# Kernel optimization log

Hardware: AMD Instinct MI355X
Metric: run time of the kernel (lower is better)

The kernel has to match this reference:

```python
import jax, jax.numpy as jnp
import numpy as np

P = 16            # num_patches = 224 // 14
T = P * P         # patches per image (256)
K = 5             # top-k templates
SIM_THR = 0.05
PATCH_THR = 2.0


def _idx2loc(idx):
    # flat patch index -> (w, h) float location, matching convert_index2location
    return jnp.stack([(idx % P).astype(jnp.float32), (idx // P).astype(jnp.float32)], axis=-1)


def setup_inputs() -> dict:
    key = jax.random.key(0)
    k1, k2, k3, k4 = jax.random.split(key, 4)
    B, N, C = 8, 32, 768
    src_feats = jax.random.normal(k1, (B, N, C, P, P), dtype=jnp.float32)
    tar_feat = jax.random.normal(k2, (B, C, P, P), dtype=jnp.float32)
    src_masks = (jax.random.uniform(k3, (B, N, P, P)) > 0.3).astype(jnp.float32)
    tar_mask = (jax.random.uniform(k4, (B, P, P)) > 0.3).astype(jnp.float32)
    return {"src_feats": src_feats, "tar_feat": tar_feat,
            "src_masks": src_masks, "tar_mask": tar_mask}


def reference(src_feats, tar_feat, src_masks, tar_mask):
    B, N, C = src_feats.shape[:3]
    # masks are already at feature resolution -> interpolate is identity; flatten
    tarm = tar_mask.reshape(B, T)                                   # (B, T)
    srcm = src_masks.reshape(B, N, T)                               # (B, N, T)
    # L2-normalize features over channel dim (F.normalize)
    tf = tar_feat / jnp.clip(jnp.linalg.norm(tar_feat, axis=1, keepdims=True), 1e-12)
    tf = tf.reshape(B, C, T)                                        # (B, C, T)
    sf = src_feats / jnp.clip(jnp.linalg.norm(src_feats, axis=2, keepdims=True), 1e-12)
    sf = sf.reshape(B, N, C, T)                                     # (B, N, C, S)
    # dense cosine similarity, masked, then thresholded to 0
    sim = jnp.einsum('bct,bncs->bnts', tf, sf)                      # (B, N, T, S)
    sim = sim * srcm[:, :, None, :] * tarm[:, None, :, None]
    sim = jnp.where(sim < SIM_THR, 0.0, sim)
    # dual nearest-neighbor search ('tar2src' direction)
    score_t2s = sim.max(axis=3)                                     # (B, N, T)
    idx_t2s = sim.argmax(axis=3).astype(jnp.int32)
    score_s2t = sim.max(axis=2)                                     # (B, N, S)
    idx_s2t = sim.argmax(axis=2).astype(jnp.int32)
    mask_sim = score_t2s >= SIM_THR
    # cycle consistency: tar -> src -> tar
    idx_s2s = jnp.take_along_axis(idx_s2t, idx_t2s, axis=2)         # (B, N, T)
    dist = jnp.linalg.norm(_idx2loc(idx_s2s) - _idx2loc(jnp.arange(T))[None, None], axis=-1)
    sim_s2s = jnp.take_along_axis(score_s2t, idx_t2s, axis=2)
    mask_cycle = (dist <= PATCH_THR) & (sim_s2s >= SIM_THR)
    # non-zero / in-mask filtering
    mask_t2s = jnp.take_along_axis(srcm, idx_t2s, axis=2)           # (B, N, T)
    mask_nz = tarm[:, None, :] * mask_t2s * (idx_s2t != 0) * (idx_t2s != 0)
    mask_all = (mask_sim & mask_cycle) * mask_nz                    # (B, N, T) float
    match_counts = mask_all.sum(axis=2)                             # (B, N)
    sim_avg = jnp.where(match_counts > 0,
                        (score_t2s * mask_all).sum(axis=2) / float(T), 0.0)
    # top-k template selection
    score_src, id_src = jax.lax.top_k(sim_avg, K)                   # (B, K)
    sel = lambda a: jnp.take_along_axis(a, id_src[:, :, None], axis=1)
    pred_mask = sel(mask_all)                                       # (B, K, T)
    score_pts = sel(score_t2s)                                      # (B, K, T)
    src_loc = _idx2loc(sel(idx_t2s)).astype(jnp.int32)              # (B, K, T, 2)
    # format_prediction: -1 outside mask, (w, h) coords inside
    grid = _idx2loc(jnp.arange(T)).astype(jnp.int32)                # (T, 2)
    nz = (pred_mask != 0)[..., None]
    tar_pts = jnp.where(nz, grid[None, None], -1)                   # (B, K, T, 2)
    src_pts = jnp.where(nz, src_loc, -1)                            # (B, K, T, 2)
    return id_src, score_src, score_pts, tar_pts, src_pts, match_counts
```

## Files before the change

kernel.cpp:

```cpp
#include <hip/hip_runtime.h>

#define T_PATCH 256
#define C_DIM   768
#define NCH     48
#define N_B     8
#define N_N     32

typedef unsigned short u16;
typedef u16   u16x8  __attribute__((ext_vector_type(8)));
typedef short s16x8  __attribute__((ext_vector_type(8)));
typedef float f32x16 __attribute__((ext_vector_type(16)));

__device__ __forceinline__ unsigned rne16(unsigned u) {
    return (u + 0x7fffu + ((u >> 16) & 1u)) >> 16;
}

__device__ __forceinline__ void split3(float x, u16& o0, u16& o1, u16& o2) {
    unsigned u0 = rne16(__float_as_uint(x));
    float f0 = __uint_as_float(u0 << 16);
    float r1 = x - f0;
    unsigned u1 = rne16(__float_as_uint(r1));
    float f1 = __uint_as_float(u1 << 16);
    float r2 = r1 - f1;
    o0 = (u16)u0; o1 = (u16)u1; o2 = (u16)(__float_as_uint(r2) >> 16);
}

__global__ void tar_split_kernel(const float* __restrict__ tar,
                                 u16* __restrict__ tS0, u16* __restrict__ tS1,
                                 u16* __restrict__ tS2, float* __restrict__ partT) {
    int blk = blockIdx.x;
    int b = blk / NCH, c = blk - b * NCH;
    int tid = threadIdx.x;
    int g = tid >> 8, t = tid & 255;
    const float* tb = tar + (size_t)b * C_DIM * T_PATCH;
    float ss = 0.f;
    u16x8 v0, v1, v2;
    #pragma unroll
    for (int j = 0; j < 8; ++j) {
        float x = tb[(c * 16 + g * 8 + j) * T_PATCH + t];
        u16 a, bb, cc;
        split3(x, a, bb, cc);
        v0[j] = a; v1[j] = bb; v2[j] = cc;
        ss = fmaf(x, x, ss);
    }
    size_t off = ((size_t)blk * 512 + tid) * 8;
    *(u16x8*)(tS0 + off) = v0;
    *(u16x8*)(tS1 + off) = v1;
    *(u16x8*)(tS2 + off) = v2;
    __shared__ float sq[512];
    sq[tid] = ss;
    __syncthreads();
    if (tid < 256) partT[blk * 256 + tid] = sq[tid] + sq[tid + 256];
}

__global__ void invt_kernel(const float* __restrict__ partT,
                            const float* __restrict__ tar_mask,
                            float* __restrict__ w_invT) {
    int b = blockIdx.x, t = threadIdx.x;
    float s = 0.f;
    for (int c = 0; c < NCH; ++c) s += partT[(b * NCH + c) * 256 + t];
    float tm = tar_mask[b * 256 + t];
    w_invT[b * 256 + t] = (tm != 0.f) ? 1.f / fmaxf(sqrtf(s), 1e-12f) : 0.f;
}

__launch_bounds__(512, 4)
__global__ void sim_kernel(const float* __restrict__ src_feats,
                           const u16* __restrict__ tS0, const u16* __restrict__ tS1,
                           const u16* __restrict__ tS2,
                           const float* __restrict__ w_invT,
                           const float* __restrict__ src_masks,
                           float* __restrict__ w_rowv, int* __restrict__ w_rowi,
                           float* __restrict__ w_s2tv, int* __restrict__ w_s2ti) {
    __shared__ __align__(16) u16 B0[2][2][128][8], B1[2][2][128][8], B2[2][2][128][8];
    __shared__ float sqS[2][128];
    __shared__ float rowv[2][256]; __shared__ int rowi[2][256];
    __shared__ float colv[4][128]; __shared__ int coli[4][128];
    __shared__ float invT[256], invS[128];

    int bh = blockIdx.x;
    int b    = bh & 7;
    int loc  = bh >> 3;
    int n    = loc >> 1;
    int half = loc & 1;
    int bn   = b * N_N + n;
    int lbh  = bn * 2 + half;

    int tid = threadIdx.x;
    int lane = tid & 63, w = tid >> 6;
    int wm = w >> 1, wn = w & 1;
    int h = lane >> 5, l5 = lane & 31;
    int colB = tid & 127, gB = (tid >> 7) & 1;

    const float* sB = src_feats + (size_t)bn * C_DIM * T_PATCH
                    + (size_t)gB * 8 * T_PATCH + half * 128 + colB;
    size_t aoff = ((size_t)b * NCH) * 4096 + (size_t)(h * 256 + wm * 64 + l5) * 8;
    const u16* pa0 = tS0 + aoff;
    const u16* pa1 = tS1 + aoff;
    const u16* pa2 = tS2 + aoff;

    if (tid < 256) invT[tid] = w_invT[b * 256 + tid];

    f32x16 acc[2][2];
    #pragma unroll
    for (int i = 0; i < 2; ++i)
        #pragma unroll
        for (int j = 0; j < 2; ++j) acc[i][j] = (f32x16)0.0f;

    float sss = 0.f;

    if (tid < 256) {
        u16x8 b0v, b1v, b2v;
        #pragma unroll
        for (int j = 0; j < 8; ++j) {
            float x = sB[j * T_PATCH];
            u16 a, bb, cc;
            split3(x, a, bb, cc);
            b0v[j] = a; b1v[j] = bb; b2v[j] = cc;
            sss = fmaf(x, x, sss);
        }
        ((u16x8*)B0[0])[tid] = b0v;
        ((u16x8*)B1[0])[tid] = b1v;
        ((u16x8*)B2[0])[tid] = b2v;
    }
    const float* psrc = sB + 4096;
    __syncthreads();

    for (int c = 0; c < NCH; ++c) {
        int p = c & 1;
        s16x8 a0[2], a1[2], a2[2];
        #pragma unroll
        for (int i = 0; i < 2; ++i) {
            a0[i] = *(const s16x8*)(pa0 + i * 256);
            a1[i] = *(const s16x8*)(pa1 + i * 256);
            a2[i] = *(const s16x8*)(pa2 + i * 256);
        }
        pa0 += 4096; pa1 += 4096; pa2 += 4096;

        float yv[8];
        bool pf = (c < NCH - 1);
        if (tid < 256 && pf) {
            #pragma unroll
            for (int j = 0; j < 8; ++j) yv[j] = psrc[j * T_PATCH];
            psrc += 4096;
        }

        __builtin_amdgcn_s_setprio(1);
        #pragma unroll
        for (int j = 0; j < 2; ++j) {
            int cl = wn * 64 + j * 32 + l5;
            s16x8 b0 = *(const s16x8*)&B0[p][h][cl][0];
            s16x8 b1 = *(const s16x8*)&B1[p][h][cl][0];
            s16x8 b2 = *(const s16x8*)&B2[p][h][cl][0];
            #pragma unroll
            for (int i = 0; i < 2; ++i) {
                acc[i][j] = __builtin_amdgcn_mfma_f32_32x32x16_bf16(a0[i], b0, acc[i][j], 0, 0, 0);
                acc[i][j] = __builtin_amdgcn_mfma_f32_32x32x16_bf16(a0[i], b1, acc[i][j], 0, 0, 0);
                acc[i][j] = __builtin_amdgcn_mfma_f32_32x32x16_bf16(a1[i], b0, acc[i][j], 0, 0, 0);
                acc[i][j] = __builtin_amdgcn_mfma_f32_32x32x16_bf16(a1[i], b1, acc[i][j], 0, 0, 0);
                acc[i][j] = __builtin_amdgcn_mfma_f32_32x32x16_bf16(a0[i], b2, acc[i][j], 0, 0, 0);
                acc[i][j] = __builtin_amdgcn_mfma_f32_32x32x16_bf16(a2[i], b0, acc[i][j], 0, 0, 0);
            }
        }
        __builtin_amdgcn_s_setprio(0);

        if (tid < 256 && pf) {
            u16x8 b0v, b1v, b2v;
            #pragma unroll
            for (int j = 0; j < 8; ++j) {
                u16 a, bb, cc;
                split3(yv[j], a, bb, cc);
                b0v[j] = a; b1v[j] = bb; b2v[j] = cc;
                sss = fmaf(yv[j], yv[j], sss);
            }
            ((u16x8*)B0[p ^ 1])[tid] = b0v;
            ((u16x8*)B1[p ^ 1])[tid] = b1v;
            ((u16x8*)B2[p ^ 1])[tid] = b2v;
        }
        __syncthreads();
    }

    if (tid < 256) ((float*)sqS)[tid] = sss;
    __syncthreads();
    if (tid < 128) {
        float ns = sqrtf(sqS[0][tid] + sqS[1][tid]);
        float smv = src_masks[bn * 256 + half * 128 + tid];
        invS[tid] = (smv != 0.f) ? 1.f / fmaxf(ns, 1e-12f) : 0.f;
    }
    __syncthreads();

    float isv[2]; int sgl[2];
    #pragma unroll
    for (int j = 0; j < 2; ++j) {
        isv[j] = invS[wn * 64 + j * 32 + l5];
        sgl[j] = half * 128 + wn * 64 + j * 32 + l5;
    }
    float cbv[2]; int cbi[2];
    #pragma unroll
    for (int j = 0; j < 2; ++j) { cbv[j] = -1.f; cbi[j] = 0; }

    #pragma unroll
    for (int i = 0; i < 2; ++i) {
        #pragma unroll
        for (int r = 0; r < 16; ++r) {
            int trow = wm * 64 + i * 32 + (r & 3) + 8 * (r >> 2) + 4 * h;
            float it = invT[trow];
            float v[2];
            #pragma unroll
            for (int j = 0; j < 2; ++j) {
                float x = acc[i][j][r] * it * isv[j];
                v[j] = (x >= 0.05f) ? x : 0.f;
            }
            float bv = -1.f; int bi = 0;
            #pragma unroll
            for (int j = 0; j < 2; ++j)
                if (v[j] > bv) { bv = v[j]; bi = sgl[j]; }
            #pragma unroll
            for (int off = 1; off < 32; off <<= 1) {
                float ov = __shfl_xor(bv, off, 64);
                int   oi = __shfl_xor(bi, off, 64);
                if (ov > bv || (ov == bv && oi < bi)) { bv = ov; bi = oi; }
            }
            if (l5 == 0) { rowv[wn][trow] = bv; rowi[wn][trow] = bi; }
            #pragma unroll
            for (int j = 0; j < 2; ++j)
                if (v[j] > cbv[j]) { cbv[j] = v[j]; cbi[j] = trow; }
        }
    }
    #pragma unroll
    for (int j = 0; j < 2; ++j) {
        float bv = cbv[j]; int bi = cbi[j];
        float ov = __shfl_xor(bv, 32, 64);
        int   oi = __shfl_xor(bi, 32, 64);
        if (ov > bv || (ov == bv && oi < bi)) { bv = ov; bi = oi; }
        if (h == 0) { colv[wm][wn * 64 + j * 32 + l5] = bv; coli[wm][wn * 64 + j * 32 + l5] = bi; }
    }
    __syncthreads();
    if (tid < 256) {
        float v0 = rowv[0][tid]; int i0 = rowi[0][tid];
        float v1 = rowv[1][tid]; int i1 = rowi[1][tid];
        if (v1 > v0 || (v1 == v0 && i1 < i0)) { v0 = v1; i0 = i1; }
        w_rowv[lbh * 256 + tid] = v0;
        w_rowi[lbh * 256 + tid] = i0;
    }
    if (tid < 128) {
        float bv = colv[0][tid]; int bi = coli[0][tid];
        #pragma unroll
        for (int q = 1; q < 4; ++q) {
            float ov = colv[q][tid]; int oi = coli[q][tid];
            if (ov > bv || (ov == bv && oi < bi)) { bv = ov; bi = oi; }
        }
        w_s2tv[bn * 256 + half * 128 + tid] = bv;
        w_s2ti[bn * 256 + half * 128 + tid] = bi;
    }
}

__global__ void combine_kernel(const float* __restrict__ w_rowv, const int* __restrict__ w_rowi,
                               const float* __restrict__ w_s2tv, const int* __restrict__ w_s2ti,
                               const float* __restrict__ src_masks, const float* __restrict__ tar_mask,
                               float* __restrict__ w_score, float* __restrict__ w_mall,
                               float* __restrict__ w_savg, int* __restrict__ w_idx,
                               float* __restrict__ out) {
    int bn = blockIdx.x; int b = bn >> 5; int t = threadIdx.x;
    __shared__ float sc_s2t[256]; __shared__ int ix_s2t[256];
    __shared__ float sm[256];
    __shared__ float red[8];
    sc_s2t[t] = w_s2tv[bn * 256 + t];
    ix_s2t[t] = w_s2ti[bn * 256 + t];
    sm[t]     = src_masks[bn * 256 + t];
    float v0 = w_rowv[(bn * 2) * 256 + t];     int i0 = w_rowi[(bn * 2) * 256 + t];
    float v1 = w_rowv[(bn * 2 + 1) * 256 + t]; int i1 = w_rowi[(bn * 2 + 1) * 256 + t];
    float st2s; int i;
    if (v1 > v0 || (v1 == v0 && i1 < i0)) { st2s = v1; i = i1; }
    else                                  { st2s = v0; i = i0; }
    float tmv = tar_mask[b * 256 + t];
    __syncthreads();

    bool msim = st2s >= 0.05f;
    int is2s = ix_s2t[i];
    int dw = (is2s & 15) - (t & 15);
    int dh = (is2s >> 4) - (t >> 4);
    bool cyc = (dw * dw + dh * dh <= 4) && (sc_s2t[i] >= 0.05f);
    float mnz = tmv * sm[i] *
                ((ix_s2t[t] != 0) ? 1.f : 0.f) *
                ((i != 0) ? 1.f : 0.f);
    float mall = (msim && cyc) ? mnz : 0.f;
    w_score[bn * 256 + t] = st2s;
    w_mall[bn * 256 + t]  = mall;
    w_idx[bn * 256 + t]   = i;

    float cnt = mall, svs = st2s * mall;
    #pragma unroll
    for (int off = 1; off < 64; off <<= 1) {
        cnt += __shfl_xor(cnt, off, 64);
        svs += __shfl_xor(svs, off, 64);
    }
    if ((t & 63) == 0) {
        red[(t >> 6) * 2]     = cnt;
        red[(t >> 6) * 2 + 1] = svs;
    }
    __syncthreads();
    if (t == 0) {
        float c = red[0] + red[2] + red[4] + red[6];
        float s = red[1] + red[3] + red[5] + red[7];
        w_savg[bn] = (c > 0.f) ? (s * (1.f / 256.f)) : 0.f;
        out[51280 + bn] = c;
    }
}

__global__ void final_kernel(const float* __restrict__ w_score,
                             const float* __restrict__ w_mall,
                             const float* __restrict__ w_savg,
                             const int*   __restrict__ w_idx,
                             float* __restrict__ out) {
    int b = blockIdx.x, tid = threadIdx.x;
    __shared__ float savg[32];
    __shared__ int   topid[5];
    __shared__ float topv[5];
    if (tid < 32) savg[tid] = w_savg[b * 32 + tid];
    __syncthreads();
    if (tid == 0) {
        unsigned used = 0;
        for (int k = 0; k < 5; ++k) {
            float bv = -1e30f; int bi = 0;
            for (int n = 0; n < 32; ++n) {
                if (!((used >> n) & 1u) && savg[n] > bv) { bv = savg[n]; bi = n; }
            }
            used |= (1u << bi);
            topid[k] = bi; topv[k] = bv;
        }
    }
    __syncthreads();
    if (tid < 5) {
        out[b * 5 + tid]      = (float)topid[tid];
        out[40 + b * 5 + tid] = topv[tid];
    }
    int t = tid;
    for (int k = 0; k < 5; ++k) {
        int bn = b * 32 + topid[k];
        float sc = w_score[bn * 256 + t];
        float ma = w_mall[bn * 256 + t];
        int   ii = w_idx[bn * 256 + t];
        int o = (b * 5 + k) * 256 + t;
        out[80 + o] = sc;
        bool nz = (ma != 0.f);
        out[10320 + 2 * o]     = nz ? (float)(t & 15)  : -1.f;
        out[10320 + 2 * o + 1] = nz ? (float)(t >> 4)  : -1.f;
        out[30800 + 2 * o]     = nz ? (float)(ii & 15) : -1.f;
        out[30800 + 2 * o + 1] = nz ? (float)(ii >> 4) : -1.f;
    }
}

extern "C" void kernel_launch(void* const* d_in, const int* in_sizes, int n_in,
                              void* d_out, int out_size, void* d_ws, size_t ws_size,
                              hipStream_t stream) {
    const float* src_feats = (const float*)d_in[0];
    const float* tar_feat  = (const float*)d_in[1];
    const float* src_masks = (const float*)d_in[2];
    const float* tar_mask  = (const float*)d_in[3];
    float* out = (float*)d_out;

    const size_t PLANE = (size_t)N_B * NCH * 512 * 8;
    u16* tS0 = (u16*)d_ws;
    u16* tS1 = tS0 + PLANE;
    u16* tS2 = tS1 + PLANE;
    float* partT  = (float*)(tS2 + PLANE);
    float* w_invT = partT + (size_t)N_B * NCH * 256;
    float* w_rowv = w_invT + 2048;
    int*   w_rowi = (int*)(w_rowv + 512 * 256);
    float* w_s2tv = (float*)(w_rowi + 512 * 256);
    int*   w_s2ti = (int*)(w_s2tv + 256 * 256);
    float* w_score = (float*)(w_s2ti + 256 * 256);
    float* w_mall  = w_score + 256 * 256;
    float* w_savg  = w_mall + 256 * 256;
    int*   w_idx   = (int*)(w_savg + 256);

    tar_split_kernel<<<N_B * NCH, 512, 0, stream>>>(tar_feat, tS0, tS1, tS2, partT);
    invt_kernel<<<N_B, 256, 0, stream>>>(partT, tar_mask, w_invT);
    sim_kernel<<<N_B * N_N * 2, 512, 0, stream>>>(src_feats, tS0, tS1, tS2, w_invT,
                                                  src_masks,
                                                  w_rowv, w_rowi, w_s2tv, w_s2ti);
    combine_kernel<<<N_B * N_N, 256, 0, stream>>>(w_rowv, w_rowi, w_s2tv, w_s2ti,
                                                  src_masks, tar_mask,
                                                  w_score, w_mall, w_savg, w_idx, out);
    final_kernel<<<N_B, 256, 0, stream>>>(w_score, w_mall, w_savg, w_idx, out);
}
```

Before: 391.8 us.

## Stage target A-tiles in LDS via async global_load_lds and split B-fill across all threads

The sim kernel now copies the pre-split target bf16 tiles straight from global memory into double-buffered LDS with global_load_lds, one 16-byte load per thread per split. Before, each wave read them from global into registers inside the MFMA loop. The source-feature split work is spread over all 512 threads at 4 channels each, where only 256 threads handled 8 each, and the norm partials are reduced over four groups. This aims to overlap A-tile fetches with compute and halve per-thread conversion latency. The cost is roughly 72KB of LDS per block, which may limit occupancy below the launch-bounds target of 4 blocks.

```diff
diff --git a/kernel.cpp b/kernel.cpp
--- a/kernel.cpp
+++ b/kernel.cpp
@@ -8,6 +8,7 @@
 
 typedef unsigned short u16;
 typedef u16   u16x8  __attribute__((ext_vector_type(8)));
+typedef u16   u16x4  __attribute__((ext_vector_type(4)));
 typedef short s16x8  __attribute__((ext_vector_type(8)));
 typedef float f32x16 __attribute__((ext_vector_type(16)));
 
@@ -23,6 +24,12 @@
     float f1 = __uint_as_float(u1 << 16);
     float r2 = r1 - f1;
     o0 = (u16)u0; o1 = (u16)u1; o2 = (u16)(__float_as_uint(r2) >> 16);
+}
+
+__device__ __forceinline__ void gll16(const u16* g, u16* l) {
+    __builtin_amdgcn_global_load_lds(
+        (const __attribute__((address_space(1))) unsigned int*)g,
+        (__attribute__((address_space(3))) unsigned int*)l, 16, 0, 0);
 }
 
 __global__ void tar_split_kernel(const float* __restrict__ tar,
@@ -71,11 +78,20 @@
                            const float* __restrict__ src_masks,
                            float* __restrict__ w_rowv, int* __restrict__ w_rowi,
                            float* __restrict__ w_s2tv, int* __restrict__ w_s2ti) {
-    __shared__ __align__(16) u16 B0[2][2][128][8], B1[2][2][128][8], B2[2][2][128][8];
-    __shared__ float sqS[2][128];
-    __shared__ float rowv[2][256]; __shared__ int rowi[2][256];
-    __shared__ float colv[4][128]; __shared__ int coli[4][128];
-    __shared__ float invT[256], invS[128];
+    __shared__ __align__(16) u16 SM[36864];
+    u16* Af0 = SM;
+    u16* Af1 = SM + 8192;
+    u16* Af2 = SM + 16384;
+    u16* Bf0 = SM + 24576;
+    u16* Bf1 = SM + 28672;
+    u16* Bf2 = SM + 32768;
+    float* sqv  = (float*)(SM);
+    float* rowv = (float*)(SM + 1024);
+    int*   rowi = (int*)  (SM + 3072);
+    float* colv = (float*)(SM + 5120);
+    int*   coli = (int*)  (SM + 6144);
+    float* invT = (float*)(SM + 7168);
+    float* invS = (float*)(SM + 7680);
 
     int bh = blockIdx.x;
     int b    = bh & 7;
@@ -89,16 +105,15 @@
     int lane = tid & 63, w = tid >> 6;
     int wm = w >> 1, wn = w & 1;
     int h = lane >> 5, l5 = lane & 31;
-    int colB = tid & 127, gB = (tid >> 7) & 1;
-
-    const float* sB = src_feats + (size_t)bn * C_DIM * T_PATCH
-                    + (size_t)gB * 8 * T_PATCH + half * 128 + colB;
-    size_t aoff = ((size_t)b * NCH) * 4096 + (size_t)(h * 256 + wm * 64 + l5) * 8;
-    const u16* pa0 = tS0 + aoff;
-    const u16* pa1 = tS1 + aoff;
-    const u16* pa2 = tS2 + aoff;
-
-    if (tid < 256) invT[tid] = w_invT[b * 256 + tid];
+    int colB = tid & 127, qB = tid >> 7;
+    int gq = qB >> 1, quad = qB & 1;
+
+    const float* psrc = src_feats + (size_t)bn * C_DIM * T_PATCH
+                      + (size_t)(gq * 8 + quad * 4) * T_PATCH + half * 128 + colB;
+    size_t abase = (size_t)b * NCH * 4096 + (size_t)tid * 8;
+    const u16* pga0 = tS0 + abase;
+    const u16* pga1 = tS1 + abase;
+    const u16* pga2 = tS2 + abase;
 
     f32x16 acc[2][2];
     #pragma unroll
@@ -108,49 +123,67 @@
 
     float sss = 0.f;
 
-    if (tid < 256) {
-        u16x8 b0v, b1v, b2v;
-        #pragma unroll
-        for (int j = 0; j < 8; ++j) {
-            float x = sB[j * T_PATCH];
+    {
+        float yv[4];
+        #pragma unroll
+        for (int j = 0; j < 4; ++j) yv[j] = psrc[j * T_PATCH];
+        psrc += 4096;
+        gll16(pga0, Af0 + tid * 8);
+        gll16(pga1, Af1 + tid * 8);
+        gll16(pga2, Af2 + tid * 8);
+        pga0 += 4096; pga1 += 4096; pga2 += 4096;
+        u16x4 b0v, b1v, b2v;
+        #pragma unroll
+        for (int j = 0; j < 4; ++j) {
             u16 a, bb, cc;
-            split3(x, a, bb, cc);
+            split3(yv[j], a, bb, cc);
             b0v[j] = a; b1v[j] = bb; b2v[j] = cc;
-            sss = fmaf(x, x, sss);
-        }
-        ((u16x8*)B0[0])[tid] = b0v;
-        ((u16x8*)B1[0])[tid] = b1v;
-        ((u16x8*)B2[0])[tid] = b2v;
-    }
-    const float* psrc = sB + 4096;
+            sss = fmaf(yv[j], yv[j], sss);
+        }
+        int bslot = (gq * 128 + colB) * 8 + quad * 4;
+        *(u16x4*)(Bf0 + bslot) = b0v;
+        *(u16x4*)(Bf1 + bslot) = b1v;
+        *(u16x4*)(Bf2 + bslot) = b2v;
+    }
     __syncthreads();
 
     for (int c = 0; c < NCH; ++c) {
         int p = c & 1;
+        bool pf = (c < NCH - 1);
+
+        float yv[4];
+        if (pf) {
+            #pragma unroll
+            for (int j = 0; j < 4; ++j) yv[j] = psrc[j * T_PATCH];
+            psrc += 4096;
+        }
+        if (pf) {
+            int adst = (p ^ 1) * 4096 + tid * 8;
+            gll16(pga0, Af0 + adst);
+            gll16(pga1, Af1 + adst);
+            gll16(pga2, Af2 + adst);
+            pga0 += 4096; pga1 += 4096; pga2 += 4096;
+        }
+
+        __builtin_amdgcn_s_setprio(1);
         s16x8 a0[2], a1[2], a2[2];
-        #pragma unroll
-        for (int i = 0; i < 2; ++i) {
-            a0[i] = *(const s16x8*)(pa0 + i * 256);
-            a1[i] = *(const s16x8*)(pa1 + i * 256);
-            a2[i] = *(const s16x8*)(pa2 + i * 256);
-        }
-        pa0 += 4096; pa1 += 4096; pa2 += 4096;
-
-        float yv[8];
-        bool pf = (c < NCH - 1);
-        if (tid < 256 && pf) {
-            #pragma unroll
-            for (int j = 0; j < 8; ++j) yv[j] = psrc[j * T_PATCH];
-            psrc += 4096;
-        }
-
-        __builtin_amdgcn_s_setprio(1);
+        {
+            const u16* Ab = Af0 + p * 4096 + (h * 256 + wm * 64 + l5) * 8;
+            #pragma unroll
+            for (int i = 0; i < 2; ++i) a0[i] = *(const s16x8*)(Ab + i * 256);
+            Ab = Af1 + p * 4096 + (h * 256 + wm * 64 + l5) * 8;
+            #pragma unroll
+            for (int i = 0; i < 2; ++i) a1[i] = *(const s16x8*)(Ab + i * 256);
+            Ab = Af2 + p * 4096 + (h * 256 + wm * 64 + l5) * 8;
+            #pragma unroll
+            for (int i = 0; i < 2; ++i) a2[i] = *(const s16x8*)(Ab + i * 256);
+        }
         #pragma unroll
         for (int j = 0; j < 2; ++j) {
-            int cl = wn * 64 + j * 32 + l5;
-            s16x8 b0 = *(const s16x8*)&B0[p][h][cl][0];
-            s16x8 b1 = *(const s16x8*)&B1[p][h][cl][0];
-            s16x8 b2 = *(const s16x8*)&B2[p][h][cl][0];
+            int boff = p * 2048 + (h * 128 + wn * 64 + j * 32 + l5) * 8;
+            s16x8 b0 = *(const s16x8*)(Bf0 + boff);
+            s16x8 b1 = *(const s16x8*)(Bf1 + boff);
+            s16x8 b2 = *(const s16x8*)(Bf2 + boff);
             #pragma unroll
             for (int i = 0; i < 2; ++i) {
                 acc[i][j] = __builtin_amdgcn_mfma_f32_32x32x16_bf16(a0[i], b0, acc[i][j], 0, 0, 0);
@@ -163,26 +196,28 @@
         }
         __builtin_amdgcn_s_setprio(0);
 
-        if (tid < 256 && pf) {
-            u16x8 b0v, b1v, b2v;
-            #pragma unroll
-            for (int j = 0; j < 8; ++j) {
+        if (pf) {
+            u16x4 b0v, b1v, b2v;
+            #pragma unroll
+            for (int j = 0; j < 4; ++j) {
                 u16 a, bb, cc;
                 split3(yv[j], a, bb, cc);
                 b0v[j] = a; b1v[j] = bb; b2v[j] = cc;
                 sss = fmaf(yv[j], yv[j], sss);
             }
-            ((u16x8*)B0[p ^ 1])[tid] = b0v;
-            ((u16x8*)B1[p ^ 1])[tid] = b1v;
-            ((u16x8*)B2[p ^ 1])[tid] = b2v;
+            int bslot = (p ^ 1) * 2048 + (gq * 128 + colB) * 8 + quad * 4;
+            *(u16x4*)(Bf0 + bslot) = b0v;
+            *(u16x4*)(Bf1 + bslot) = b1v;
+            *(u16x4*)(Bf2 + bslot) = b2v;
         }
         __syncthreads();
     }
 
-    if (tid < 256) ((float*)sqS)[tid] = sss;
+    sqv[tid] = sss;
+    if (tid < 256) invT[tid] = w_invT[b * 256 + tid];
     __syncthreads();
     if (tid < 128) {
-        float ns = sqrtf(sqS[0][tid] + sqS[1][tid]);
+        float ns = sqrtf(sqv[tid] + sqv[tid + 128] + sqv[tid + 256] + sqv[tid + 384]);
         float smv = src_masks[bn * 256 + half * 128 + tid];
         invS[tid] = (smv != 0.f) ? 1.f / fmaxf(ns, 1e-12f) : 0.f;
     }
@@ -220,7 +255,7 @@
                 int   oi = __shfl_xor(bi, off, 64);
                 if (ov > bv || (ov == bv && oi < bi)) { bv = ov; bi = oi; }
             }
-            if (l5 == 0) { rowv[wn][trow] = bv; rowi[wn][trow] = bi; }
+            if (l5 == 0) { rowv[wn * 256 + trow] = bv; rowi[wn * 256 + trow] = bi; }
             #pragma unroll
             for (int j = 0; j < 2; ++j)
                 if (v[j] > cbv[j]) { cbv[j] = v[j]; cbi[j] = trow; }
@@ -232,21 +267,22 @@
         float ov = __shfl_xor(bv, 32, 64);
         int   oi = __shfl_xor(bi, 32, 64);
         if (ov > bv || (ov == bv && oi < bi)) { bv = ov; bi = oi; }
-        if (h == 0) { colv[wm][wn * 64 + j * 32 + l5] = bv; coli[wm][wn * 64 + j * 32 + l5] = bi; }
+        if (h == 0) { colv[wm * 128 + wn * 64 + j * 32 + l5] = bv;
+                      coli[wm * 128 + wn * 64 + j * 32 + l5] = bi; }
     }
     __syncthreads();
     if (tid < 256) {
-        float v0 = rowv[0][tid]; int i0 = rowi[0][tid];
-        float v1 = rowv[1][tid]; int i1 = rowi[1][tid];
+        float v0 = rowv[tid];       int i0 = rowi[tid];
+        float v1 = rowv[256 + tid]; int i1 = rowi[256 + tid];
         if (v1 > v0 || (v1 == v0 && i1 < i0)) { v0 = v1; i0 = i1; }
         w_rowv[lbh * 256 + tid] = v0;
         w_rowi[lbh * 256 + tid] = i0;
     }
     if (tid < 128) {
-        float bv = colv[0][tid]; int bi = coli[0][tid];
+        float bv = colv[tid]; int bi = coli[tid];
         #pragma unroll
         for (int q = 1; q < 4; ++q) {
-            float ov = colv[q][tid]; int oi = coli[q][tid];
+            float ov = colv[q * 128 + tid]; int oi = coli[q * 128 + tid];
             if (ov > bv || (ov == bv && oi < bi)) { bv = ov; bi = oi; }
         }
         w_s2tv[bn * 256 + half * 128 + tid] = bv;
```

Result: faster. 372.6 us (-4.9%).
